# Performance work log

Hardware: AMD Instinct MI355X
Metric: run time of the kernel (lower is better)

The kernel has to match this reference:

```python
import jax, jax.numpy as jnp
import numpy as np

NDIM = 1024
NTOKEN = 50257
CUTOFFS = [2000, 10000, NTOKEN]  # cutoffs + [ntoken]
DIV = 4
N = 4096
HEAD_SIZE = CUTOFFS[0] + len(CUTOFFS) - 1  # 2002


def setup_inputs() -> dict:
    key = jax.random.key(0)
    ks = jax.random.split(key, 8)
    inputs = jax.random.normal(ks[0], (N, NDIM), dtype=jnp.float32)
    targets = jax.random.randint(ks[1], (N,), 0, NTOKEN, dtype=jnp.int32)
    # head: nn.Linear(ndim, head_size, bias=False) -> weight [head_size, ndim], xavier
    def xavier(k, shape):
        fan_out, fan_in = shape
        lim = np.sqrt(6.0 / (fan_in + fan_out))
        return jax.random.uniform(k, shape, jnp.float32, -lim, lim)
    head_W = xavier(ks[2], (HEAD_SIZE, NDIM))
    # tail cluster 0: size 8000, low dim 256; cluster 1: size 40257, low dim 64
    sz0 = CUTOFFS[1] - CUTOFFS[0]
    sz1 = CUTOFFS[2] - CUTOFFS[1]
    d0, d1 = NDIM // DIV, NDIM // DIV**2
    emb0 = jax.random.normal(ks[3], (sz0, d0), dtype=jnp.float32) * d0 ** -0.5
    emb1 = jax.random.normal(ks[4], (sz1, d1), dtype=jnp.float32) * d1 ** -0.5
    lin0 = xavier(ks[5], (NDIM, d0))  # nn.Linear(d0, ndim).weight
    lin1 = xavier(ks[6], (NDIM, d1))
    return {"inputs": inputs, "targets": targets, "head_W": head_W,
            "emb0": emb0, "lin0": lin0, "emb1": emb1, "lin1": lin1}


def _adaptive_logprob(inputs, targets, head_W, emb0, lin0, emb1, lin1):
    tails = [(emb0, lin0), (emb1, lin1)]
    # map targets -> head targets (in-head id, or cluster slot cutoffs[0]+i)
    head_targets = targets
    masks = []
    for i in range(len(tails)):
        m = (targets >= CUTOFFS[i]) & (targets < CUTOFFS[i + 1])
        masks.append(m)
        head_targets = jnp.where(m, CUTOFFS[0] + i, head_targets)
    # head: logits [N, head_size], gather per-row log-prob
    head_lp = jax.nn.log_softmax(inputs @ head_W.T, axis=-1)
    out = jnp.take_along_axis(head_lp, head_targets[:, None], axis=1)[:, 0]
    # tails: logits = (x @ lin) @ emb^T (low-rank), log-softmax, masked gather
    for i, (emb, lin) in enumerate(tails):
        size = CUTOFFS[i + 1] - CUTOFFS[i]
        lp = jax.nn.log_softmax((inputs @ lin) @ emb.T, axis=-1)  # [N, size]
        rel = jnp.clip(targets - CUTOFFS[i], 0, size - 1)
        g = jnp.take_along_axis(lp, rel[:, None], axis=1)[:, 0]
        out = out + jnp.where(masks[i], g, 0.0)
    return out


def reference(inputs, targets, head_W, emb0, lin0, emb1, lin1):
    outputs = _adaptive_logprob(inputs, targets, head_W, emb0, lin0, emb1, lin1)
    loss = (-outputs).mean()
    return outputs, loss
```

## Files before the change

kernel.cpp:

```cpp
#include <hip/hip_runtime.h>


typedef __attribute__((ext_vector_type(8))) short short8;
typedef __attribute__((ext_vector_type(4))) float f32x4;

#define LOG2E 1.4426950408889634f
#define LN2   0.6931471805599453f

__device__ __forceinline__ float b2f(unsigned short u){
    return __uint_as_float(((unsigned int)u) << 16);
}
__device__ __forceinline__ unsigned short f2b(float f){
    unsigned int x = __float_as_uint(f);
    x += 0x7fffu + ((x >> 16) & 1u);
    return (unsigned short)(x >> 16);
}
__device__ __forceinline__ float dotu(unsigned int xu, unsigned int wu){
    float a = __uint_as_float(xu << 16) * __uint_as_float(wu << 16);
    float b = __uint_as_float(xu & 0xffff0000u) * __uint_as_float(wu & 0xffff0000u);
    return a + b;
}
__device__ __forceinline__ float fexp2(float x){
#if __has_builtin(__builtin_amdgcn_exp2f)
    return __builtin_amdgcn_exp2f(x);
#else
    float r; asm("v_exp_f32 %0, %1" : "=v"(r) : "v"(x)); return r;
#endif
}
__device__ __forceinline__ void gload16(const unsigned short* g, unsigned short* l){
    __builtin_amdgcn_global_load_lds(
        (const __attribute__((address_space(1))) unsigned int*)g,
        (__attribute__((address_space(3))) unsigned int*)l, 16, 0, 0);
}

__global__ __launch_bounds__(256) void k_prep(
    const float* __restrict__ X, const float* __restrict__ headW,
    const float* __restrict__ emb0, const float* __restrict__ emb1,
    const float* __restrict__ lin0, const float* __restrict__ lin1,
    unsigned short* __restrict__ Xb, unsigned short* __restrict__ hWb,
    unsigned short* __restrict__ e0b, unsigned short* __restrict__ e1b,
    unsigned short* __restrict__ l0T, unsigned short* __restrict__ l1T,
    float* __restrict__ sums)
{
    __shared__ unsigned short tileT[64][65];
    const int b = blockIdx.x, t = threadIdx.x;
    if (b < 80){
        const float* src; unsigned short* dst; int C, tx, ty;
        if (b < 64){ src = lin0; dst = l0T; C = 256; tx = b & 3; ty = b >> 2; }
        else       { src = lin1; dst = l1T; C = 64;  tx = 0;     ty = b - 64; }
        #pragma unroll
        for (int e = 0; e < 16; ++e){
            int idx = t + e*256, r = idx >> 6, c = idx & 63;
            tileT[c][r] = f2b(src[(ty*64 + r)*C + tx*64 + c]);
        }
        __syncthreads();
        #pragma unroll
        for (int e = 0; e < 16; ++e){
            int idx = t + e*256, cc = idx >> 6, rr = idx & 63;
            dst[(tx*64 + cc)*1024 + ty*64 + rr] = tileT[cc][rr];
        }
        return;
    }
    const int NX = 1048576, NH = 512512, NE0 = 512000, NE1 = 644112;
    const int NV = NX + NH + NE0 + NE1;
    const int NS = 12288;
    const int total = NV + NS;
    int stride = (gridDim.x - 80) * blockDim.x;
    for (int i = (b - 80)*blockDim.x + t; i < total; i += stride){
        if (i < NV){
            const float* src; unsigned short* dst; int off; float sc;
            if (i < NX)            { src = X;     dst = Xb;  off = i;           sc = 1.0f;  }
            else if (i < NX+NH)    { src = headW; dst = hWb; off = i-NX;        sc = LOG2E; }
            else if (i < NX+NH+NE0){ src = emb0;  dst = e0b; off = i-NX-NH;     sc = LOG2E; }
            else                   { src = emb1;  dst = e1b; off = i-NX-NH-NE0; sc = LOG2E; }
            float4 v = ((const float4*)src)[off];
            ushort4 o;
            o.x = f2b(v.x*sc); o.y = f2b(v.y*sc);
            o.z = f2b(v.z*sc); o.w = f2b(v.w*sc);
            ((ushort4*)dst)[off] = o;
        } else {
            sums[i - NV] = 0.f;
        }
    }
}

__global__ __launch_bounds__(256) void k_hgemm(
    const unsigned short* __restrict__ A,
    const unsigned short* __restrict__ B0, unsigned short* __restrict__ C0,
    const unsigned short* __restrict__ B1, unsigned short* __restrict__ C1)
{
    constexpr int K = 1024;
    __shared__ __align__(16) unsigned short As[64*64];
    __shared__ __align__(16) unsigned short Bs[64*64];

    const int yy = blockIdx.y;
    const unsigned short* B = (yy < 4) ? B0 : B1;
    unsigned short* C = (yy < 4) ? C0 : C1;
    const int M  = (yy < 4) ? 256 : 64;
    const int cb = (yy < 4) ? yy : 0;

    const int tid  = threadIdx.x;
    const int lane = tid & 63;
    const int w    = tid >> 6;
    const int waveR = w >> 1, waveC = w & 1;
    const int quad  = lane >> 4, l16 = lane & 15;
    const int row0  = blockIdx.x * 64;

    f32x4 acc[2][2];
    #pragma unroll
    for (int i = 0; i < 2; ++i)
    #pragma unroll
    for (int j = 0; j < 2; ++j)
        acc[i][j] = (f32x4){0.f, 0.f, 0.f, 0.f};

    for (int kc = 0; kc < K/64; ++kc){
        __syncthreads();
        #pragma unroll
        for (int it = 0; it < 2; ++it){
            int idx = tid + it*256;
            int r = idx >> 3, g = idx & 7;
            *((uint4*)&As[r*64 + ((g ^ (r & 7)) << 3)]) =
                *(const uint4*)(A + (row0 + r)*K + kc*64 + g*8);
            *((uint4*)&Bs[r*64 + ((g ^ (r & 7)) << 3)]) =
                *(const uint4*)(B + (cb*64 + r)*K + kc*64 + g*8);
        }
        __syncthreads();
        #pragma unroll
        for (int ks = 0; ks < 2; ++ks){
            short8 a[2], b[2];
            #pragma unroll
            for (int i = 0; i < 2; ++i){
                int r = waveR*32 + i*16 + l16;
                int g = ks*4 + quad;
                a[i] = *(const short8*)&As[r*64 + ((g ^ (r & 7)) << 3)];
            }
            #pragma unroll
            for (int j = 0; j < 2; ++j){
                int r = waveC*32 + j*16 + l16;
                int g = ks*4 + quad;
                b[j] = *(const short8*)&Bs[r*64 + ((g ^ (r & 7)) << 3)];
            }
            #pragma unroll
            for (int i = 0; i < 2; ++i)
            #pragma unroll
            for (int j = 0; j < 2; ++j)
                acc[i][j] = __builtin_amdgcn_mfma_f32_16x16x32_bf16(
                    a[i], b[j], acc[i][j], 0, 0, 0);
        }
    }
    #pragma unroll
    for (int i = 0; i < 2; ++i)
    #pragma unroll
    for (int j = 0; j < 2; ++j)
    #pragma unroll
    for (int r = 0; r < 4; ++r){
        int row = row0 + waveR*32 + i*16 + quad*4 + r;
        int col = cb*64 + waveC*32 + j*16 + l16;
        C[row*M + col] = f2b(acc[i][j][r]);
    }
}

template<int K>
__device__ __forceinline__ void sumexp_lds(
    const unsigned short* __restrict__ A,
    const unsigned short* __restrict__ B,
    float* __restrict__ s_out, int M,
    int rowb, int cb0, int cb1,
    unsigned short* __restrict__ As,
    unsigned short* __restrict__ Bs)
{
    constexpr int KCH = K / 64;
    constexpr int LK  = (KCH == 16) ? 4 : 2;
    static_assert(KCH == 16 || KCH == 4, "");
    const int tid  = threadIdx.x;
    const int lane = tid & 63, w = tid >> 6;
    const int waveR = w >> 1, waveC = w & 1;
    const int quad  = lane >> 4, l16 = lane & 15;
    const int row0  = rowb * 64;
    const int nit   = (cb1 - cb0) << LK;

    float s_loc[8];
    #pragma unroll
    for (int i = 0; i < 8; ++i) s_loc[i] = 0.f;
    f32x4 acc[2][2];
    #pragma unroll
    for (int i = 0; i < 2; ++i)
    #pragma unroll
    for (int j = 0; j < 2; ++j) acc[i][j] = (f32x4){0.f,0.f,0.f,0.f};

    const int sr = w*16 + (lane >> 3);
    const int gk = ((lane & 7) ^ (sr & 7)) << 3;

    int aoff[2][2], boff[2][2];
    #pragma unroll
    for (int x = 0; x < 2; ++x)
    #pragma unroll
    for (int ks = 0; ks < 2; ++ks){
        int ra = waveR*32 + x*16 + l16;
        int rb = waveC*32 + x*16 + l16;
        int g  = ks*4 + quad;
        aoff[x][ks] = ra*64 + ((g ^ (ra & 7)) << 3);
        boff[x][ks] = rb*64 + ((g ^ (rb & 7)) << 3);
    }

    auto stage = [&](int it){
        int cb = cb0 + (it >> LK);
        int kc = it & (KCH - 1);
        unsigned short* Ad = As + (it & 1)*4096 + w*1024;
        unsigned short* Bd = Bs + (it & 1)*4096 + w*1024;
        const unsigned short* ga = A + (size_t)(row0 + sr)*K + kc*64 + gk;
        gload16(ga,        Ad);
        gload16(ga + 8*K,  Ad + 512);
        int br0 = cb*64 + sr;     if (br0 > M-1) br0 = M-1;
        int br1 = cb*64 + sr + 8; if (br1 > M-1) br1 = M-1;
        gload16(B + (size_t)br0*K + kc*64 + gk, Bd);
        gload16(B + (size_t)br1*K + kc*64 + gk, Bd + 512);
    };

    stage(0);
    __syncthreads();

    for (int it = 0; it < nit; ++it){
        if (it + 1 < nit) stage(it + 1);
        const unsigned short* Ac = As + (it & 1)*4096;
        const unsigned short* Bc = Bs + (it & 1)*4096;
        #pragma unroll
        for (int ks = 0; ks < 2; ++ks){
            short8 a0 = *(const short8*)(Ac + aoff[0][ks]);
            short8 a1 = *(const short8*)(Ac + aoff[1][ks]);
            short8 b0 = *(const short8*)(Bc + boff[0][ks]);
            short8 b1 = *(const short8*)(Bc + boff[1][ks]);
            acc[0][0] = __builtin_amdgcn_mfma_f32_16x16x32_bf16(a0, b0, acc[0][0], 0,0,0);
            acc[0][1] = __builtin_amdgcn_mfma_f32_16x16x32_bf16(a0, b1, acc[0][1], 0,0,0);
            acc[1][0] = __builtin_amdgcn_mfma_f32_16x16x32_bf16(a1, b0, acc[1][0], 0,0,0);
            acc[1][1] = __builtin_amdgcn_mfma_f32_16x16x32_bf16(a1, b1, acc[1][1], 0,0,0);
        }
        if ((it & (KCH - 1)) == (KCH - 1)){
            int cb = cb0 + (it >> LK);
            if ((cb + 1)*64 <= M){
                #pragma unroll
                for (int i = 0; i < 2; ++i)
                #pragma unroll
                for (int j = 0; j < 2; ++j)
                #pragma unroll
                for (int r = 0; r < 4; ++r)
                    s_loc[i*4 + r] += fexp2(acc[i][j][r]);
            } else {
                #pragma unroll
                for (int j = 0; j < 2; ++j){
                    int col = cb*64 + waveC*32 + j*16 + l16;
                    if (col < M){
                        #pragma unroll
                        for (int i = 0; i < 2; ++i)
                        #pragma unroll
                        for (int r = 0; r < 4; ++r)
                            s_loc[i*4 + r] += fexp2(acc[i][j][r]);
                    }
                }
            }
            #pragma unroll
            for (int i = 0; i < 2; ++i)
            #pragma unroll
            for (int j = 0; j < 2; ++j) acc[i][j] = (f32x4){0.f,0.f,0.f,0.f};
        }
        __syncthreads();
    }

    #pragma unroll
    for (int k = 0; k < 8; ++k){
        #pragma unroll
        for (int m = 1; m < 16; m <<= 1)
            s_loc[k] += __shfl_xor(s_loc[k], m, 64);
    }
    if (l16 < 8){
        int i = l16 >> 2, r = l16 & 3;
        int row = row0 + waveR*32 + i*16 + quad*4 + r;
        atomicAdd(&s_out[row], s_loc[l16]);
    }
}

__device__ __forceinline__ void sumexp_stream64(
    const unsigned short* __restrict__ A,
    const unsigned short* __restrict__ B,
    float* __restrict__ s_out, int wid)
{
    const int M = 40257;
    const int lane = threadIdx.x & 63;
    const int quad = lane >> 4, l16 = lane & 15;
    const int rowg  = wid >> 6;
    const int split = wid & 63;
    const int g0 = split*39 + min(split, 21);
    const int g1 = g0 + 39 + (split < 21 ? 1 : 0);
    const int row0 = rowg * 64;

    short8 a[4][2];
    #pragma unroll
    for (int i = 0; i < 4; ++i)
    #pragma unroll
    for (int ks = 0; ks < 2; ++ks)
        a[i][ks] = *(const short8*)(A + (row0 + i*16 + l16)*64 + ks*32 + quad*8);

    f32x4 sums[4];
    #pragma unroll
    for (int i = 0; i < 4; ++i) sums[i] = (f32x4){0.f,0.f,0.f,0.f};

    short8 p0a, p1a, p0b, p1b;
    auto loadB = [&](int g, short8& d0, short8& d1){
        int n = g*16 + l16; if (n > M-1) n = M-1;
        const unsigned short* p = B + n*64 + quad*8;
        d0 = *(const short8*)p;
        d1 = *(const short8*)(p + 32);
    };
    auto body = [&](int g, short8 b0, short8 b1){
        f32x4 acc[4];
        #pragma unroll
        for (int i = 0; i < 4; ++i) acc[i] = (f32x4){0.f,0.f,0.f,0.f};
        #pragma unroll
        for (int i = 0; i < 4; ++i)
            acc[i] = __builtin_amdgcn_mfma_f32_16x16x32_bf16(a[i][0], b0, acc[i], 0,0,0);
        #pragma unroll
        for (int i = 0; i < 4; ++i)
            acc[i] = __builtin_amdgcn_mfma_f32_16x16x32_bf16(a[i][1], b1, acc[i], 0,0,0);
        if (g*16 + l16 < M){
            #pragma unroll
            for (int i = 0; i < 4; ++i){
                sums[i][0] += fexp2(acc[i][0]);
                sums[i][1] += fexp2(acc[i][1]);
                sums[i][2] += fexp2(acc[i][2]);
                sums[i][3] += fexp2(acc[i][3]);
            }
        }
    };

    loadB(g0, p0a, p1a);
    loadB(g0 + 1, p0b, p1b);
    for (int g = g0; g < g1; g += 2){
        body(g, p0a, p1a);
        if (g + 2 < g1) loadB(g + 2, p0a, p1a);
        if (g + 1 < g1){
            body(g + 1, p0b, p1b);
            if (g + 3 < g1) loadB(g + 3, p0b, p1b);
        }
    }

    #pragma unroll
    for (int i = 0; i < 4; ++i){
        #pragma unroll
        for (int r = 0; r < 4; ++r){
            float v = sums[i][r];
            v += __shfl_xor(v, 1, 64);
            v += __shfl_xor(v, 2, 64);
            v += __shfl_xor(v, 4, 64);
            v += __shfl_xor(v, 8, 64);
            if (l16 == 0)
                atomicAdd(&s_out[row0 + i*16 + quad*4 + r], v);
        }
    }
}

__global__ __launch_bounds__(256) void k_sumexp(
    const unsigned short* __restrict__ Xb,  const unsigned short* __restrict__ hWb,
    const unsigned short* __restrict__ h0b, const unsigned short* __restrict__ e0b,
    const unsigned short* __restrict__ h1b, const unsigned short* __restrict__ e1b,
    float* __restrict__ sH, float* __restrict__ s0, float* __restrict__ s1)
{
    __shared__ __align__(16) unsigned short As[2*4096];
    __shared__ __align__(16) unsigned short Bs[2*4096];
    const int b = blockIdx.x;
    const int m4 = b & 3;
    if (m4 == 0){
        int id = b >> 2, rowb = id >> 3, split = id & 7;
        sumexp_lds<1024>(Xb, hWb, sH, 2002, rowb, split*4, split*4 + 4, As, Bs);
    } else if (m4 == 2){
        int id = b >> 2, rowb = id >> 3, split = id & 7;
        int cb0 = split*15 + min(split, 5);
        int cb1 = cb0 + 15 + (split < 5 ? 1 : 0);
        sumexp_lds<256>(h0b, e0b, s0, 8000, rowb, cb0, cb1, As, Bs);
    } else {
        int wid = (b >> 1)*4 + (threadIdx.x >> 6);
        sumexp_stream64(h1b, e1b, s1, wid);
    }
}

__global__ __launch_bounds__(256) void k_combine(
    const unsigned short* __restrict__ Xb,   const unsigned short* __restrict__ hWb,
    const unsigned short* __restrict__ h0b,  const unsigned short* __restrict__ e0b,
    const unsigned short* __restrict__ h1b,  const unsigned short* __restrict__ e1b,
    const float* __restrict__ sH, const float* __restrict__ s0,
    const float* __restrict__ s1,
    const int* __restrict__ targets, float* __restrict__ out)
{
    int w = threadIdx.x >> 6, lane = threadIdx.x & 63;
    int row = blockIdx.x*4 + w;
    int t = targets[row];
    int hidx = t < 2000 ? t : (t < 10000 ? 2000 : 2001);
    int rel0 = min(max(t - 2000, 0), 7999);
    int rel1 = min(max(t - 10000, 0), 40256);

    float dh = 0.f;
    {
        const uint4* xa = (const uint4*)(Xb  + row*1024  + lane*16);
        const uint4* wb = (const uint4*)(hWb + hidx*1024 + lane*16);
        #pragma unroll
        for (int p = 0; p < 2; ++p){
            uint4 xv = xa[p], wv = wb[p];
            dh += dotu(xv.x, wv.x) + dotu(xv.y, wv.y)
                + dotu(xv.z, wv.z) + dotu(xv.w, wv.w);
        }
    }
    float d0;
    {
        uint2 xv = *(const uint2*)(h0b + row*256  + lane*4);
        uint2 wv = *(const uint2*)(e0b + rel0*256 + lane*4);
        d0 = dotu(xv.x, wv.x) + dotu(xv.y, wv.y);
    }
    float d1 = b2f(h1b[row*64 + lane]) * b2f(e1b[rel1*64 + lane]);

    #pragma unroll
    for (int m = 1; m < 64; m <<= 1){
        dh += __shfl_xor(dh, m, 64);
        d0 += __shfl_xor(d0, m, 64);
        d1 += __shfl_xor(d1, m, 64);
    }
    if (lane == 0){
        float lp = dh - log2f(sH[row]);
        if (t >= 2000 && t < 10000) lp += d0 - log2f(s0[row]);
        if (t >= 10000)             lp += d1 - log2f(s1[row]);
        out[row] = LN2 * lp;
    }
}

__global__ void k_loss(const float* __restrict__ out, float* __restrict__ loss){
    __shared__ float red[1024];
    float s = 0.f;
    for (int i = threadIdx.x; i < 4096; i += 1024) s += out[i];
    red[threadIdx.x] = s;
    __syncthreads();
    for (int ofs = 512; ofs > 0; ofs >>= 1){
        if (threadIdx.x < ofs) red[threadIdx.x] += red[threadIdx.x + ofs];
        __syncthreads();
    }
    if (threadIdx.x == 0) loss[0] = -red[0] / 4096.f;
}

extern "C" void kernel_launch(void* const* d_in, const int* in_sizes, int n_in,
                              void* d_out, int out_size, void* d_ws, size_t ws_size,
                              hipStream_t stream) {
    const float* X      = (const float*)d_in[0];
    const int*   tgt    = (const int*)  d_in[1];
    const float* headW  = (const float*)d_in[2];
    const float* emb0   = (const float*)d_in[3];
    const float* lin0   = (const float*)d_in[4];
    const float* emb1   = (const float*)d_in[5];
    const float* lin1   = (const float*)d_in[6];
    float* out = (float*)d_out;

    char* ws = (char*)d_ws;
    unsigned short* Xb  = (unsigned short*)(ws + 0);
    unsigned short* hWb = (unsigned short*)(ws + 8388608);
    unsigned short* e0b = (unsigned short*)(ws + 12488704);
    unsigned short* e1b = (unsigned short*)(ws + 16584704);
    unsigned short* l0T = (unsigned short*)(ws + 21737600);
    unsigned short* l1T = (unsigned short*)(ws + 22261888);
    unsigned short* h0b = (unsigned short*)(ws + 22392960);
    unsigned short* h1b = (unsigned short*)(ws + 24490112);
    float* sums         = (float*)(ws + 25014400);
    float* sH = sums, *s0 = sums + 4096, *s1 = sums + 8192;

    k_prep<<<2048, 256, 0, stream>>>(X, headW, emb0, emb1, lin0, lin1,
                                     Xb, hWb, e0b, e1b, l0T, l1T, sums);
    k_hgemm<<<dim3(64, 5), 256, 0, stream>>>(Xb, l0T, h0b, l1T, h1b);
    k_sumexp<<<2048, 256, 0, stream>>>(Xb, hWb, h0b, e0b, h1b, e1b, sH, s0, s1);
    k_combine<<<1024, 256, 0, stream>>>(Xb, hWb, h0b, e0b, h1b, e1b,
                                        sH, s0, s1, tgt, out);
    k_loss<<<1, 1024, 0, stream>>>(out, out + 4096);
}
```

Baseline: 235.4 us.

## Compact rows by target cluster so tail GEMMs and sum-exp run only on needed rows

The prep kernel now bins rows by target cluster, using atomic counters to build compacted index lists and per-row positions. The tail projection GEMM and the tail sum-exp passes then run only over row bands holding rows whose target falls in that cluster, writing sums back through the index list. This removes tail work whose results the reference masks out anyway. The separate loss kernel is folded into the combine kernel through an atomic accumulator and a last-block ticket, and a memset replaces the in-kernel zeroing. The atomic binning makes row order nondeterministic, and blocks for skipped bands simply exit, so the remaining blocks are not rebalanced.

Result: slower. 243.9 us (+3.6%).

```diff
diff --git a/kernel.cpp b/kernel.cpp
--- a/kernel.cpp
+++ b/kernel.cpp
@@ -37,10 +37,12 @@
     const float* __restrict__ X, const float* __restrict__ headW,
     const float* __restrict__ emb0, const float* __restrict__ emb1,
     const float* __restrict__ lin0, const float* __restrict__ lin1,
+    const int* __restrict__ tgt,
     unsigned short* __restrict__ Xb, unsigned short* __restrict__ hWb,
     unsigned short* __restrict__ e0b, unsigned short* __restrict__ e1b,
     unsigned short* __restrict__ l0T, unsigned short* __restrict__ l1T,
-    float* __restrict__ sums)
+    int* __restrict__ idx0, int* __restrict__ idx1,
+    int* __restrict__ pos0, int* __restrict__ pos1, int* __restrict__ cnt)
 {
     __shared__ unsigned short tileT[64][65];
     const int b = blockIdx.x, t = threadIdx.x;
@@ -63,10 +65,9 @@
     }
     const int NX = 1048576, NH = 512512, NE0 = 512000, NE1 = 644112;
     const int NV = NX + NH + NE0 + NE1;
-    const int NS = 12288;
-    const int total = NV + NS;
-    int stride = (gridDim.x - 80) * blockDim.x;
-    for (int i = (b - 80)*blockDim.x + t; i < total; i += stride){
+    const int total = NV + 4096;
+    int stride = (gridDim.x - 80) * 256;
+    for (int i = (b - 80)*256 + t; i < total; i += stride){
         if (i < NV){
             const float* src; unsigned short* dst; int off; float sc;
             if (i < NX)            { src = X;     dst = Xb;  off = i;           sc = 1.0f;  }
@@ -79,7 +80,15 @@
             o.z = f2b(v.z*sc); o.w = f2b(v.w*sc);
             ((ushort4*)dst)[off] = o;
         } else {
-            sums[i - NV] = 0.f;
+            int row = i - NV;
+            int tv = tgt[row];
+            int p0 = 0, p1 = 0;
+            if (tv >= 2000 && tv < 10000){
+                int p = atomicAdd(&cnt[0], 1); idx0[p] = row; p0 = p;
+            } else if (tv >= 10000){
+                int p = atomicAdd(&cnt[1], 1); idx1[p] = row; p1 = p;
+            }
+            pos0[row] = p0; pos1[row] = p1;
         }
     }
 }
@@ -87,76 +96,84 @@
 __global__ __launch_bounds__(256) void k_hgemm(
     const unsigned short* __restrict__ A,
     const unsigned short* __restrict__ B0, unsigned short* __restrict__ C0,
-    const unsigned short* __restrict__ B1, unsigned short* __restrict__ C1)
+    const unsigned short* __restrict__ B1, unsigned short* __restrict__ C1,
+    const int* __restrict__ idx0, const int* __restrict__ idx1,
+    const int* __restrict__ cnt)
 {
     constexpr int K = 1024;
     __shared__ __align__(16) unsigned short As[64*64];
     __shared__ __align__(16) unsigned short Bs[64*64];
 
-    const int yy = blockIdx.y;
-    const unsigned short* B = (yy < 4) ? B0 : B1;
-    unsigned short* C = (yy < 4) ? C0 : C1;
-    const int M  = (yy < 4) ? 256 : 64;
-    const int cb = (yy < 4) ? yy : 0;
+    const int j = blockIdx.x;
+    const bool isH0 = (j < 256);
+    const int band = isH0 ? (j >> 2) : (j - 256);
+    const int cntv = isH0 ? cnt[0] : cnt[1];
+    if (band >= ((cntv + 63) >> 6)) return;
+    const unsigned short* B = isH0 ? B0 : B1;
+    unsigned short* C = isH0 ? C0 : C1;
+    const int M  = isH0 ? 256 : 64;
+    const int cb = isH0 ? (j & 3) : 0;
+    const int* idx = isH0 ? idx0 : idx1;
 
     const int tid  = threadIdx.x;
     const int lane = tid & 63;
     const int w    = tid >> 6;
     const int waveR = w >> 1, waveC = w & 1;
     const int quad  = lane >> 4, l16 = lane & 15;
-    const int row0  = blockIdx.x * 64;
+
+    const int r0l = tid >> 3, r1l = r0l + 32, g = tid & 7;
+    const int gr0 = idx[min(band*64 + r0l, cntv - 1)];
+    const int gr1 = idx[min(band*64 + r1l, cntv - 1)];
 
     f32x4 acc[2][2];
     #pragma unroll
     for (int i = 0; i < 2; ++i)
     #pragma unroll
-    for (int j = 0; j < 2; ++j)
-        acc[i][j] = (f32x4){0.f, 0.f, 0.f, 0.f};
+    for (int jj = 0; jj < 2; ++jj) acc[i][jj] = (f32x4){0.f,0.f,0.f,0.f};
 
     for (int kc = 0; kc < K/64; ++kc){
         __syncthreads();
-        #pragma unroll
-        for (int it = 0; it < 2; ++it){
-            int idx = tid + it*256;
-            int r = idx >> 3, g = idx & 7;
-            *((uint4*)&As[r*64 + ((g ^ (r & 7)) << 3)]) =
-                *(const uint4*)(A + (row0 + r)*K + kc*64 + g*8);
-            *((uint4*)&Bs[r*64 + ((g ^ (r & 7)) << 3)]) =
-                *(const uint4*)(B + (cb*64 + r)*K + kc*64 + g*8);
-        }
+        *((uint4*)&As[r0l*64 + ((g ^ (r0l & 7)) << 3)]) =
+            *(const uint4*)(A + (size_t)gr0*K + kc*64 + g*8);
+        *((uint4*)&As[r1l*64 + ((g ^ (r1l & 7)) << 3)]) =
+            *(const uint4*)(A + (size_t)gr1*K + kc*64 + g*8);
+        *((uint4*)&Bs[r0l*64 + ((g ^ (r0l & 7)) << 3)]) =
+            *(const uint4*)(B + (size_t)(cb*64 + r0l)*K + kc*64 + g*8);
+        *((uint4*)&Bs[r1l*64 + ((g ^ (r1l & 7)) << 3)]) =
+            *(const uint4*)(B + (size_t)(cb*64 + r1l)*K + kc*64 + g*8);
         __syncthreads();
         #pragma unroll
         for (int ks = 0; ks < 2; ++ks){
-            short8 a[2], b[2];
+            short8 a[2], bb[2];
             #pragma unroll
             for (int i = 0; i < 2; ++i){
                 int r = waveR*32 + i*16 + l16;
-                int g = ks*4 + quad;
-                a[i] = *(const short8*)&As[r*64 + ((g ^ (r & 7)) << 3)];
+                int gg = ks*4 + quad;
+                a[i] = *(const short8*)&As[r*64 + ((gg ^ (r & 7)) << 3)];
             }
             #pragma unroll
-            for (int j = 0; j < 2; ++j){
-                int r = waveC*32 + j*16 + l16;
-                int g = ks*4 + quad;
-                b[j] = *(const short8*)&Bs[r*64 + ((g ^ (r & 7)) << 3)];
+            for (int jj = 0; jj < 2; ++jj){
+                int r = waveC*32 + jj*16 + l16;
+                int gg = ks*4 + quad;
+                bb[jj] = *(const short8*)&Bs[r*64 + ((gg ^ (r & 7)) << 3)];
             }
             #pragma unroll
             for (int i = 0; i < 2; ++i)
             #pragma unroll
-            for (int j = 0; j < 2; ++j)
-                acc[i][j] = __builtin_amdgcn_mfma_f32_16x16x32_bf16(
-                    a[i], b[j], acc[i][j], 0, 0, 0);
+            for (int jj = 0; jj < 2; ++jj)
+                acc[i][jj] = __builtin_amdgcn_mfma_f32_16x16x32_bf16(
+                    a[i], bb[jj], acc[i][jj], 0, 0, 0);
         }
     }
     #pragma unroll
     for (int i = 0; i < 2; ++i)
     #pragma unroll
-    for (int j = 0; j < 2; ++j)
+    for (int jj = 0; jj < 2; ++jj)
     #pragma unroll
     for (int r = 0; r < 4; ++r){
-        int row = row0 + waveR*32 + i*16 + quad*4 + r;
-        int col = cb*64 + waveC*32 + j*16 + l16;
-        C[row*M + col] = f2b(acc[i][j][r]);
+        int crow = band*64 + waveR*32 + i*16 + quad*4 + r;
+        int col  = cb*64 + waveC*32 + jj*16 + l16;
+        C[crow*M + col] = f2b(acc[i][jj][r]);
     }
 }
 
@@ -166,8 +183,8 @@
     const unsigned short* __restrict__ B,
     float* __restrict__ s_out, int M,
     int rowb, int cb0, int cb1,
-    unsigned short* __restrict__ As,
-    unsigned short* __restrict__ Bs)
+    unsigned short* __restrict__ As, unsigned short* __restrict__ Bs,
+    const int* __restrict__ idx, int cnt)
 {
     constexpr int KCH = K / 64;
     constexpr int LK  = (KCH == 16) ? 4 : 2;
@@ -274,31 +291,31 @@
     }
     if (l16 < 8){
         int i = l16 >> 2, r = l16 & 3;
-        int row = row0 + waveR*32 + i*16 + quad*4 + r;
-        atomicAdd(&s_out[row], s_loc[l16]);
+        int lrow = row0 + waveR*32 + i*16 + quad*4 + r;
+        if (idx){
+            if (lrow < cnt) atomicAdd(&s_out[idx[lrow]], s_loc[l16]);
+        } else {
+            atomicAdd(&s_out[lrow], s_loc[l16]);
+        }
     }
 }
 
 __device__ __forceinline__ void sumexp_stream64(
     const unsigned short* __restrict__ A,
     const unsigned short* __restrict__ B,
-    float* __restrict__ s_out, int wid)
+    float* __restrict__ s_out, int row0, int g0, int g1,
+    const int* __restrict__ idx, int cnt)
 {
     const int M = 40257;
     const int lane = threadIdx.x & 63;
     const int quad = lane >> 4, l16 = lane & 15;
-    const int rowg  = wid >> 6;
-    const int split = wid & 63;
-    const int g0 = split*39 + min(split, 21);
-    const int g1 = g0 + 39 + (split < 21 ? 1 : 0);
-    const int row0 = rowg * 64;
 
     short8 a[4][2];
     #pragma unroll
     for (int i = 0; i < 4; ++i)
     #pragma unroll
     for (int ks = 0; ks < 2; ++ks)
-        a[i][ks] = *(const short8*)(A + (row0 + i*16 + l16)*64 + ks*32 + quad*8);
+        a[i][ks] = *(const short8*)(A + (size_t)(row0 + i*16 + l16)*64 + ks*32 + quad*8);
 
     f32x4 sums[4];
     #pragma unroll
@@ -307,7 +324,7 @@
     short8 p0a, p1a, p0b, p1b;
     auto loadB = [&](int g, short8& d0, short8& d1){
         int n = g*16 + l16; if (n > M-1) n = M-1;
-        const unsigned short* p = B + n*64 + quad*8;
+        const unsigned short* p = B + (size_t)n*64 + quad*8;
         d0 = *(const short8*)p;
         d1 = *(const short8*)(p + 32);
     };
@@ -352,8 +369,9 @@
             v += __shfl_xor(v, 2, 64);
             v += __shfl_xor(v, 4, 64);
             v += __shfl_xor(v, 8, 64);
-            if (l16 == 0)
-                atomicAdd(&s_out[row0 + i*16 + quad*4 + r], v);
+            int orow = row0 + i*16 + quad*4 + r;
+            if (l16 == 0 && orow < cnt)
+                atomicAdd(&s_out[idx[orow]], v);
         }
     }
 }
@@ -362,7 +380,9 @@
     const unsigned short* __restrict__ Xb,  const unsigned short* __restrict__ hWb,
     const unsigned short* __restrict__ h0b, const unsigned short* __restrict__ e0b,
     const unsigned short* __restrict__ h1b, const unsigned short* __restrict__ e1b,
-    float* __restrict__ sH, float* __restrict__ s0, float* __restrict__ s1)
+    float* __restrict__ sH, float* __restrict__ s0, float* __restrict__ s1,
+    const int* __restrict__ idx0, const int* __restrict__ idx1,
+    const int* __restrict__ cnt)
 {
     __shared__ __align__(16) unsigned short As[2*4096];
     __shared__ __align__(16) unsigned short Bs[2*4096];
@@ -370,15 +390,26 @@
     const int m4 = b & 3;
     if (m4 == 0){
         int id = b >> 2, rowb = id >> 3, split = id & 7;
-        sumexp_lds<1024>(Xb, hWb, sH, 2002, rowb, split*4, split*4 + 4, As, Bs);
+        sumexp_lds<1024>(Xb, hWb, sH, 2002, rowb, split*4, split*4 + 4,
+                         As, Bs, nullptr, 4096);
     } else if (m4 == 2){
         int id = b >> 2, rowb = id >> 3, split = id & 7;
-        int cb0 = split*15 + min(split, 5);
-        int cb1 = cb0 + 15 + (split < 5 ? 1 : 0);
-        sumexp_lds<256>(h0b, e0b, s0, 8000, rowb, cb0, cb1, As, Bs);
+        int c0 = cnt[0];
+        if (rowb < ((c0 + 63) >> 6)){
+            int cb0 = split*15 + min(split, 5);
+            int cb1 = cb0 + 15 + (split < 5 ? 1 : 0);
+            sumexp_lds<256>(h0b, e0b, s0, 8000, rowb, cb0, cb1,
+                            As, Bs, idx0, c0);
+        }
     } else {
         int wid = (b >> 1)*4 + (threadIdx.x >> 6);
-        sumexp_stream64(h1b, e1b, s1, wid);
+        int rowg = wid >> 6, split = wid & 63;
+        int c1 = cnt[1];
+        if (rowg < ((c1 + 63) >> 6)){
+            int g0 = split*39 + min(split, 21);
+            int g1 = g0 + 39 + (split < 21 ? 1 : 0);
+            sumexp_stream64(h1b, e1b, s1, rowg*64, g0, g1, idx1, c1);
+        }
     }
 }
 
@@ -388,19 +419,22 @@
     const unsigned short* __restrict__ h1b,  const unsigned short* __restrict__ e1b,
     const float* __restrict__ sH, const float* __restrict__ s0,
     const float* __restrict__ s1,
-    const int* __restrict__ targets, float* __restrict__ out)
+    const int* __restrict__ targets,
+    const int* __restrict__ pos0, const int* __restrict__ pos1,
+    float* __restrict__ lossacc, int* __restrict__ ticket,
+    float* __restrict__ out)
 {
+    __shared__ float red4[4];
     int w = threadIdx.x >> 6, lane = threadIdx.x & 63;
     int row = blockIdx.x*4 + w;
     int t = targets[row];
     int hidx = t < 2000 ? t : (t < 10000 ? 2000 : 2001);
-    int rel0 = min(max(t - 2000, 0), 7999);
-    int rel1 = min(max(t - 10000, 0), 40256);
+    int c0 = pos0[row], c1 = pos1[row];
 
     float dh = 0.f;
     {
-        const uint4* xa = (const uint4*)(Xb  + row*1024  + lane*16);
-        const uint4* wb = (const uint4*)(hWb + hidx*1024 + lane*16);
+        const uint4* xa = (const uint4*)(Xb  + (size_t)row*1024  + lane*16);
+        const uint4* wb = (const uint4*)(hWb + (size_t)hidx*1024 + lane*16);
         #pragma unroll
         for (int p = 0; p < 2; ++p){
             uint4 xv = xa[p], wv = wb[p];
@@ -408,13 +442,15 @@
                 + dotu(xv.z, wv.z) + dotu(xv.w, wv.w);
         }
     }
+    int rel0 = min(max(t - 2000, 0), 7999);
+    int rel1 = min(max(t - 10000, 0), 40256);
     float d0;
     {
-        uint2 xv = *(const uint2*)(h0b + row*256  + lane*4);
-        uint2 wv = *(const uint2*)(e0b + rel0*256 + lane*4);
+        uint2 xv = *(const uint2*)(h0b + (size_t)c0*256  + lane*4);
+        uint2 wv = *(const uint2*)(e0b + (size_t)rel0*256 + lane*4);
         d0 = dotu(xv.x, wv.x) + dotu(xv.y, wv.y);
     }
-    float d1 = b2f(h1b[row*64 + lane]) * b2f(e1b[rel1*64 + lane]);
+    float d1 = b2f(h1b[(size_t)c1*64 + lane]) * b2f(e1b[(size_t)rel1*64 + lane]);
 
     #pragma unroll
     for (int m = 1; m < 64; m <<= 1){
@@ -426,21 +462,21 @@
         float lp = dh - log2f(sH[row]);
         if (t >= 2000 && t < 10000) lp += d0 - log2f(s0[row]);
         if (t >= 10000)             lp += d1 - log2f(s1[row]);
-        out[row] = LN2 * lp;
-    }
-}
-
-__global__ void k_loss(const float* __restrict__ out, float* __restrict__ loss){
-    __shared__ float red[1024];
-    float s = 0.f;
-    for (int i = threadIdx.x; i < 4096; i += 1024) s += out[i];
-    red[threadIdx.x] = s;
+        float val = LN2 * lp;
+        out[row] = val;
+        red4[w] = val;
+    }
     __syncthreads();
-    for (int ofs = 512; ofs > 0; ofs >>= 1){
-        if (threadIdx.x < ofs) red[threadIdx.x] += red[threadIdx.x + ofs];
-        __syncthreads();
-    }
-    if (threadIdx.x == 0) loss[0] = -red[0] / 4096.f;
+    if (threadIdx.x == 0){
+        atomicAdd(lossacc, red4[0] + red4[1] + red4[2] + red4[3]);
+        __threadfence();
+        int old = atomicAdd(ticket, 1);
+        if (old == 1023){
+            __threadfence();
+            float tot = atomicAdd(lossacc, 0.0f);
+            out[4096] = -tot / 4096.f;
+        }
+    }
 }
 
 extern "C" void kernel_launch(void* const* d_in, const int* in_sizes, int n_in,
@@ -465,13 +501,24 @@
     unsigned short* h0b = (unsigned short*)(ws + 22392960);
     unsigned short* h1b = (unsigned short*)(ws + 24490112);
     float* sums         = (float*)(ws + 25014400);
+    int*   cnt          = (int*)  (ws + 25063552);
+    int*   ticket       = (int*)  (ws + 25063560);
+    float* lossacc      = (float*)(ws + 25063564);
+    int*   idx0         = (int*)  (ws + 25063568);
+    int*   idx1         = (int*)  (ws + 25079952);
+    int*   pos0         = (int*)  (ws + 25096336);
+    int*   pos1         = (int*)  (ws + 25112720);
     float* sH = sums, *s0 = sums + 4096, *s1 = sums + 8192;
 
-    k_prep<<<2048, 256, 0, stream>>>(X, headW, emb0, emb1, lin0, lin1,
-                                     Xb, hWb, e0b, e1b, l0T, l1T, sums);
-    k_hgemm<<<dim3(64, 5), 256, 0, stream>>>(Xb, l0T, h0b, l1T, h1b);
-    k_sumexp<<<2048, 256, 0, stream>>>(Xb, hWb, h0b, e0b, h1b, e1b, sH, s0, s1);
+    hipMemsetAsync(ws + 25014400, 0, 49168, stream);
+
+    k_prep<<<2048, 256, 0, stream>>>(X, headW, emb0, emb1, lin0, lin1, tgt,
+                                     Xb, hWb, e0b, e1b, l0T, l1T,
+                                     idx0, idx1, pos0, pos1, cnt);
+    k_hgemm<<<320, 256, 0, stream>>>(Xb, l0T, h0b, l1T, h1b, idx0, idx1, cnt);
+    k_sumexp<<<2048, 256, 0, stream>>>(Xb, hWb, h0b, e0b, h1b, e1b,
+                                       sH, s0, s1, idx0, idx1, cnt);
     k_combine<<<1024, 256, 0, stream>>>(Xb, hWb, h0b, e0b, h1b, e1b,
-                                        sH, s0, s1, tgt, out);
-    k_loss<<<1, 1024, 0, stream>>>(out, out + 4096);
-}
+                                        sH, s0, s1, tgt, pos0, pos1,
+                                        lossacc, ticket, out);
+}
```
